# Optimization experiments

Hardware: AMD Instinct MI355X
Metric: run time of the kernel (lower is better)

The kernel has to match this reference:

```python
import jax, jax.numpy as jnp
import numpy as np

N_NODES = 100000


def _sage_conv(x, edge_index, W_l, W_r, b):
    # PyG SAGEConv (mean aggr): out_i = lin_l(mean_{j in N(i)} x_j) + lin_r(x_i)
    src, dst = edge_index[0], edge_index[1]
    msg = x[src]  # [E, d] gather
    agg_sum = jax.ops.segment_sum(msg, dst, num_segments=N_NODES)  # [N, d]
    deg = jax.ops.segment_sum(jnp.ones((src.shape[0],), x.dtype), dst, num_segments=N_NODES)
    agg = agg_sum / jnp.maximum(deg, 1.0)[:, None]  # mean aggregation
    return agg @ W_l.T + b + x @ W_r.T


def setup_inputs() -> dict:
    key = jax.random.key(0)
    k = jax.random.split(key, 8)
    d_in, hidden, out = 64, 128, 128
    x = jax.random.normal(k[0], (N_NODES, d_in), dtype=jnp.float32)
    edge_index = jax.random.randint(k[1], (2, 1600000), 0, N_NODES, dtype=jnp.int64)
    s1 = 1.0 / np.sqrt(d_in)
    s2 = 1.0 / np.sqrt(hidden)
    return {
        "x": x,
        "edge_index": edge_index,
        "W1_l": jax.random.uniform(k[2], (hidden, d_in), jnp.float32, -s1, s1),
        "W1_r": jax.random.uniform(k[3], (hidden, d_in), jnp.float32, -s1, s1),
        "b1": jnp.zeros((hidden,), jnp.float32),
        "W2_l": jax.random.uniform(k[4], (out, hidden), jnp.float32, -s2, s2),
        "W2_r": jax.random.uniform(k[5], (out, hidden), jnp.float32, -s2, s2),
        "b2": jnp.zeros((out,), jnp.float32),
    }


def reference(x, edge_index, W1_l, W1_r, b1, W2_l, W2_r, b2):
    h = jax.nn.relu(_sage_conv(x, edge_index, W1_l, W1_r, b1))
    return _sage_conv(h, edge_index, W2_l, W2_r, b2)
```

## Files before the change

kernel.cpp:

```cpp
#include <hip/hip_runtime.h>

#define NN 100000
#define NE 1600000
#define SCAN_BLK 2048

#define BSH 9
#define NBUCK2 ((NN + 511) / 512)
#define CHUNK 8192
#define NCHK ((NE + CHUNK - 1) / CHUNK)
#define L2T (NBUCK2 * NCHK)
#define NSTRIP (NN / 32)
#define NG128 (NN / 16)

using bf16x8 = __attribute__((ext_vector_type(8))) short;
using f32x16 = __attribute__((ext_vector_type(16))) float;

__device__ __forceinline__ unsigned short f2bf(float f) {
    unsigned u = __float_as_uint(f);
    u += 0x7FFFu + ((u >> 16) & 1u);
    return (unsigned short)(u >> 16);
}
__device__ __forceinline__ float bf2f(unsigned short h) {
    return __uint_as_float(((unsigned)h) << 16);
}

__global__ __launch_bounds__(256) void hist2_kernel(const int* __restrict__ dst,
                                                    int* __restrict__ histm) {
    __shared__ int lh[256];
    int blk = blockIdx.x, tid = threadIdx.x;
    lh[tid] = 0;
    __syncthreads();
    int base = blk * CHUNK;
#pragma unroll
    for (int t = 0; t < CHUNK / 256; t++) {
        int e = base + t * 256 + tid;
        if (e < NE) atomicAdd(&lh[dst[e] >> BSH], 1);
    }
    __syncthreads();
    if (tid < NBUCK2) histm[tid * NCHK + blk] = lh[tid];
}

__global__ __launch_bounds__(256) void scan1_kernel(int* __restrict__ data,
                                                    int* __restrict__ bsums, int L) {
    __shared__ int s[256];
    int bid = blockIdx.x, tid = threadIdx.x;
    int base = bid * SCAN_BLK + tid * 8;
    int v[8];
    int sum = 0;
#pragma unroll
    for (int t = 0; t < 8; t++) {
        int idx = base + t;
        v[t] = (idx < L) ? data[idx] : 0;
        sum += v[t];
    }
    s[tid] = sum;
    __syncthreads();
    for (int off = 1; off < 256; off <<= 1) {
        int val = (tid >= off) ? s[tid - off] : 0;
        __syncthreads();
        s[tid] += val;
        __syncthreads();
    }
    int excl = s[tid] - sum;
    if (tid == 255) bsums[bid] = s[255];
    int run = excl;
#pragma unroll
    for (int t = 0; t < 8; t++) {
        int idx = base + t;
        if (idx < L) data[idx] = run;
        run += v[t];
    }
}

__global__ __launch_bounds__(64) void scan2_kernel(int* __restrict__ bsums, int n) {
    int tid = threadIdx.x;
    int orig = (tid < n) ? bsums[tid] : 0;
    int v = orig;
    for (int off = 1; off < 64; off <<= 1) {
        int nb = __shfl_up(v, off, 64);
        if (tid >= off) v += nb;
    }
    if (tid < n) bsums[tid] = v - orig;
}

__global__ __launch_bounds__(256) void scan_add_kernel(int* __restrict__ data,
                                                       const int* __restrict__ bsums, int L) {
    int i = blockIdx.x * 256 + threadIdx.x;
    if (i < L) data[i] += bsums[i / SCAN_BLK];
}

__global__ __launch_bounds__(256) void scatter2_kernel(const int* __restrict__ src,
                                                       const int* __restrict__ dst,
                                                       const int* __restrict__ histm,
                                                       int* __restrict__ tmp) {
    __shared__ int lcur[256];
    int blk = blockIdx.x, tid = threadIdx.x;
    if (tid < NBUCK2) lcur[tid] = histm[tid * NCHK + blk];
    __syncthreads();
    int base = blk * CHUNK;
#pragma unroll
    for (int t = 0; t < CHUNK / 256; t++) {
        int e = base + t * 256 + tid;
        if (e < NE) {
            int d = dst[e];
            int p = atomicAdd(&lcur[d >> BSH], 1);
            tmp[p] = src[e] | ((d & 511) << 17);
        }
    }
}

__global__ __launch_bounds__(256) void count_place_kernel(const int* __restrict__ histm,
                                                          const int* __restrict__ tmp,
                                                          int* __restrict__ rowptr,
                                                          int* __restrict__ esrc) {
    __shared__ int cnt[512];
    __shared__ int s[256];
    int b = blockIdx.x, tid = threadIdx.x;
    int beg = histm[b * NCHK];
    int end = (b == NBUCK2 - 1) ? NE : histm[(b + 1) * NCHK];

    cnt[tid] = 0; cnt[tid + 256] = 0;
    __syncthreads();
    for (int e = beg + tid; e < end; e += 256)
        atomicAdd(&cnt[tmp[e] >> 17], 1);
    __syncthreads();

    int c0 = cnt[2 * tid], c1 = cnt[2 * tid + 1];
    int sum = c0 + c1;
    s[tid] = sum;
    __syncthreads();
    for (int off = 1; off < 256; off <<= 1) {
        int val = (tid >= off) ? s[tid - off] : 0;
        __syncthreads();
        s[tid] += val;
        __syncthreads();
    }
    int o0 = beg + s[tid] - sum;
    int o1 = o0 + c0;
    cnt[2 * tid] = o0;
    cnt[2 * tid + 1] = o1;
    int node0 = (b << BSH) + 2 * tid;
    if (node0 < NN)     rowptr[node0]     = o0;
    if (node0 + 1 < NN) rowptr[node0 + 1] = o1;
    if (b == 0 && tid == 0) rowptr[NN] = NE;
    __syncthreads();

    for (int e = beg + tid; e < end; e += 256) {
        int v = tmp[e];
        int p = atomicAdd(&cnt[v >> 17], 1);
        esrc[p] = v & 0x1FFFF;
    }
}

__global__ __launch_bounds__(256) void cvt_kernel(const float* __restrict__ in,
                                                  unsigned short* __restrict__ out, int n4) {
    int i = blockIdx.x * 256 + threadIdx.x;
    if (i < n4) {
        float4 f = ((const float4*)in)[i];
        ((ushort4*)out)[i] = make_ushort4(f2bf(f.x), f2bf(f.y), f2bf(f.z), f2bf(f.w));
    }
}

__global__ __launch_bounds__(256) void agg64_kernel(const unsigned short* __restrict__ feat,
                                                    const int* __restrict__ rowptr,
                                                    const int* __restrict__ esrc,
                                                    unsigned short* __restrict__ agg) {
    int node = blockIdx.x * 4 + (threadIdx.x >> 6);
    int lane = threadIdx.x & 63;
    int es = lane >> 3;
    int fi = lane & 7;
    int beg = rowptr[node], end = rowptr[node + 1];

    float ax[8];
#pragma unroll
    for (int i = 0; i < 8; i++) ax[i] = 0.0f;

    int e = beg;
    for (; e + 15 < end; e += 16) {
        int sA = esrc[e + es];
        int sB = esrc[e + 8 + es];
        bf16x8 uA = *(const bf16x8*)(feat + (size_t)sA * 64 + fi * 8);
        bf16x8 uB = *(const bf16x8*)(feat + (size_t)sB * 64 + fi * 8);
#pragma unroll
        for (int i = 0; i < 8; i++)
            ax[i] += bf2f((unsigned short)uA[i]) + bf2f((unsigned short)uB[i]);
    }
    if (e + 7 < end) {
        int s = esrc[e + es];
        bf16x8 u = *(const bf16x8*)(feat + (size_t)s * 64 + fi * 8);
#pragma unroll
        for (int i = 0; i < 8; i++) ax[i] += bf2f((unsigned short)u[i]);
        e += 8;
    }
    if (es < end - e) {
        int s = esrc[e + es];
        bf16x8 u = *(const bf16x8*)(feat + (size_t)s * 64 + fi * 8);
#pragma unroll
        for (int i = 0; i < 8; i++) ax[i] += bf2f((unsigned short)u[i]);
    }

#pragma unroll
    for (int i = 0; i < 8; i++) {
        ax[i] += __shfl_xor(ax[i], 8);
        ax[i] += __shfl_xor(ax[i], 16);
        ax[i] += __shfl_xor(ax[i], 32);
    }
    if (es == 0) {
        float inv = 1.0f / fmaxf((float)(end - beg), 1.0f);
        bf16x8 o;
#pragma unroll
        for (int i = 0; i < 8; i++) o[i] = (short)f2bf(ax[i] * inv);
        *(bf16x8*)(agg + (size_t)node * 64 + fi * 8) = o;
    }
}

__global__ __launch_bounds__(256) void agg128_split_kernel(
    const unsigned short* __restrict__ hbT,
    const int* __restrict__ rowptr,
    const int* __restrict__ esrc,
    unsigned short* __restrict__ agg) {
    int b = blockIdx.x;
    int c = b & 7;
    int g = b >> 3;
    int tid = threadIdx.x;
    int w = tid >> 6;
    int lane = tid & 63;
    int node = g * 16 + w * 4 + (lane >> 4);
    int es = (lane >> 1) & 7;
    int fi = lane & 1;
    int beg = rowptr[node], end = rowptr[node + 1];

    const unsigned short* tab = hbT + (size_t)c * NN * 16;

    float ax[8];
#pragma unroll
    for (int i = 0; i < 8; i++) ax[i] = 0.0f;

    int e = beg + es;
    for (; e + 8 < end; e += 16) {
        int s0 = esrc[e];
        int s1 = esrc[e + 8];
        bf16x8 u0 = *(const bf16x8*)(tab + (size_t)s0 * 16 + fi * 8);
        bf16x8 u1 = *(const bf16x8*)(tab + (size_t)s1 * 16 + fi * 8);
#pragma unroll
        for (int i = 0; i < 8; i++)
            ax[i] += bf2f((unsigned short)u0[i]) + bf2f((unsigned short)u1[i]);
    }
    if (e < end) {
        int s0 = esrc[e];
        bf16x8 u0 = *(const bf16x8*)(tab + (size_t)s0 * 16 + fi * 8);
#pragma unroll
        for (int i = 0; i < 8; i++) ax[i] += bf2f((unsigned short)u0[i]);
    }

#pragma unroll
    for (int i = 0; i < 8; i++) {
        ax[i] += __shfl_xor(ax[i], 2);
        ax[i] += __shfl_xor(ax[i], 4);
        ax[i] += __shfl_xor(ax[i], 8);
    }
    if (es == 0) {
        float inv = 1.0f / fmaxf((float)(end - beg), 1.0f);
        bf16x8 o;
#pragma unroll
        for (int i = 0; i < 8; i++) o[i] = (short)f2bf(ax[i] * inv);
        *(bf16x8*)(agg + (size_t)node * 128 + c * 16 + fi * 8) = o;
    }
}

template <int K, bool RELU, bool OUTBF, bool A2SPLIT, bool OUTSPLIT>
__global__ __launch_bounds__(256) void gemm_mfma_kernel(
    const unsigned short* __restrict__ A1,
    const unsigned short* __restrict__ A2,
    const unsigned short* __restrict__ Wa,
    const unsigned short* __restrict__ Wb,
    const float* __restrict__ bias,
    void* __restrict__ outv) {
    int strip = blockIdx.x * 4 + (threadIdx.x >> 6);
    if (strip >= NSTRIP) return;
    const int lane = threadIdx.x & 63;
    const int m = lane & 31;
    const int half = lane >> 5;
    const int base = strip * 32;

    f32x16 acc[4];
#pragma unroll
    for (int nb = 0; nb < 4; ++nb)
#pragma unroll
        for (int r = 0; r < 16; ++r) acc[nb][r] = 0.0f;

    const unsigned short* ar1 = A1 + (size_t)(base + m) * K + half * 8;
#pragma unroll
    for (int kc = 0; kc < K; kc += 16) {
        bf16x8 a = *(const bf16x8*)(ar1 + kc);
#pragma unroll
        for (int nb = 0; nb < 4; ++nb) {
            bf16x8 b = *(const bf16x8*)(Wa + (size_t)(nb * 32 + m) * K + kc + half * 8);
            acc[nb] = __builtin_amdgcn_mfma_f32_32x32x16_bf16(a, b, acc[nb], 0, 0, 0);
        }
    }
#pragma unroll
    for (int kc = 0; kc < K; kc += 16) {
        bf16x8 a;
        if (A2SPLIT) {
            int off = kc + half * 8;
            a = *(const bf16x8*)(A2 + (size_t)(off >> 4) * NN * 16 +
                                 (size_t)(base + m) * 16 + (off & 15));
        } else {
            a = *(const bf16x8*)(A2 + (size_t)(base + m) * K + half * 8 + kc);
        }
#pragma unroll
        for (int nb = 0; nb < 4; ++nb) {
            bf16x8 b = *(const bf16x8*)(Wb + (size_t)(nb * 32 + m) * K + kc + half * 8);
            acc[nb] = __builtin_amdgcn_mfma_f32_32x32x16_bf16(a, b, acc[nb], 0, 0, 0);
        }
    }

#pragma unroll
    for (int nb = 0; nb < 4; ++nb) {
        int j = nb * 32 + m;
        float bz = bias[j];
#pragma unroll
        for (int r = 0; r < 16; ++r) {
            int row = (r & 3) + 8 * (r >> 2) + 4 * half;
            float v = acc[nb][r] + bz;
            if (RELU) v = fmaxf(v, 0.0f);
            if (OUTSPLIT) {
                size_t idx = (size_t)(j >> 4) * NN * 16 + (size_t)(base + row) * 16 + (j & 15);
                ((unsigned short*)outv)[idx] = f2bf(v);
            } else {
                size_t idx = (size_t)(base + row) * 128 + j;
                if (OUTBF) ((unsigned short*)outv)[idx] = f2bf(v);
                else       ((float*)outv)[idx] = v;
            }
        }
    }
}

extern "C" void kernel_launch(void* const* d_in, const int* in_sizes, int n_in,
                              void* d_out, int out_size, void* d_ws, size_t ws_size,
                              hipStream_t stream) {
    const float* x   = (const float*)d_in[0];
    const int*   ei  = (const int*)d_in[1];
    const float* W1l = (const float*)d_in[2];
    const float* W1r = (const float*)d_in[3];
    const float* b1  = (const float*)d_in[4];
    const float* W2l = (const float*)d_in[5];
    const float* W2r = (const float*)d_in[6];
    const float* b2  = (const float*)d_in[7];
    float* out = (float*)d_out;

    const int* src = ei;
    const int* dst = ei + NE;

    char* ws = (char*)d_ws;
    int* rowptr = (int*)ws;
    int* esrc   = (int*)(ws + 401408);
    unsigned short* aggB = (unsigned short*)(ws + 6803456);
    unsigned short* xb   = aggB + (size_t)NN * 64;
    char* E = ws + 32403456;
    unsigned short* hbT = (unsigned short*)E;
    int* tmp   = (int*)E;
    int* histm = (int*)(E + 6400000);
    int* bsums = (int*)(E + 6560000);
    unsigned short* W1lb = (unsigned short*)d_out;
    unsigned short* W1rb = W1lb + 128 * 64;
    unsigned short* W2lb = (unsigned short*)ws;
    unsigned short* W2rb = W2lb + 128 * 128;

    const int GB  = (NSTRIP + 3) / 4;
    const int NSB2 = (L2T + SCAN_BLK - 1) / SCAN_BLK;

    hist2_kernel<<<NCHK, 256, 0, stream>>>(dst, histm);
    scan1_kernel<<<NSB2, 256, 0, stream>>>(histm, bsums, L2T);
    scan2_kernel<<<1, 64, 0, stream>>>(bsums, NSB2);
    scan_add_kernel<<<(L2T + 255) / 256, 256, 0, stream>>>(histm, bsums, L2T);
    scatter2_kernel<<<NCHK, 256, 0, stream>>>(src, dst, histm, tmp);
    count_place_kernel<<<NBUCK2, 256, 0, stream>>>(histm, tmp, rowptr, esrc);

    cvt_kernel<<<(NN * 64 / 4 + 255) / 256, 256, 0, stream>>>(x, xb, NN * 64 / 4);
    cvt_kernel<<<(128 * 64 / 4 + 255) / 256, 256, 0, stream>>>(W1l, W1lb, 128 * 64 / 4);
    cvt_kernel<<<(128 * 64 / 4 + 255) / 256, 256, 0, stream>>>(W1r, W1rb, 128 * 64 / 4);

    agg64_kernel<<<NN / 4, 256, 0, stream>>>(xb, rowptr, esrc, aggB);
    gemm_mfma_kernel<64, true, true, false, true><<<GB, 256, 0, stream>>>(
        aggB, xb, W1lb, W1rb, b1, hbT);

    agg128_split_kernel<<<NG128 * 8, 256, 0, stream>>>(hbT, rowptr, esrc, aggB);
    cvt_kernel<<<(128 * 128 / 4 + 255) / 256, 256, 0, stream>>>(W2l, W2lb, 128 * 128 / 4);
    cvt_kernel<<<(128 * 128 / 4 + 255) / 256, 256, 0, stream>>>(W2r, W2rb, 128 * 128 / 4);
    gemm_mfma_kernel<128, false, false, true, false><<<GB, 256, 0, stream>>>(
        aggB, hbT, W2lb, W2rb, b2, out);
}
```

Before: 349.9 us.

## Assign one wavefront per node in split agg128 and store aggregate in split layout

The second-layer aggregation kernel now maps one wavefront per node instead of four nodes per wavefront. Each of 32 lane pairs handles a strided subset of edges, and the partial sums are reduced across the full wave. The aggregate is written in the same chunked (split) layout as the hidden table, and the second GEMM gains an A1SPLIT option to read it. This makes the stores contiguous per chunk and spreads each node's edges over more lanes. The trade-off is 4x more blocks and wasted lanes for low-degree nodes, since average degree is about 16.

```diff
diff --git a/kernel.cpp b/kernel.cpp
--- a/kernel.cpp
+++ b/kernel.cpp
@@ -10,7 +10,6 @@
 #define NCHK ((NE + CHUNK - 1) / CHUNK)
 #define L2T (NBUCK2 * NCHK)
 #define NSTRIP (NN / 32)
-#define NG128 (NN / 16)
 
 using bf16x8 = __attribute__((ext_vector_type(8))) short;
 using f32x16 = __attribute__((ext_vector_type(16))) float;
@@ -218,39 +217,25 @@
     const unsigned short* __restrict__ hbT,
     const int* __restrict__ rowptr,
     const int* __restrict__ esrc,
-    unsigned short* __restrict__ agg) {
-    int b = blockIdx.x;
-    int c = b & 7;
-    int g = b >> 3;
-    int tid = threadIdx.x;
-    int w = tid >> 6;
-    int lane = tid & 63;
-    int node = g * 16 + w * 4 + (lane >> 4);
-    int es = (lane >> 1) & 7;
+    unsigned short* __restrict__ aggT) {
+    int c = blockIdx.x & 7;
+    int node = (blockIdx.x >> 3) * 4 + (threadIdx.x >> 6);
+    int lane = threadIdx.x & 63;
+    int es = lane >> 1;
     int fi = lane & 1;
     int beg = rowptr[node], end = rowptr[node + 1];
 
-    const unsigned short* tab = hbT + (size_t)c * NN * 16;
+    const unsigned short* tab = hbT + (size_t)c * NN * 16 + fi * 8;
 
     float ax[8];
 #pragma unroll
     for (int i = 0; i < 8; i++) ax[i] = 0.0f;
 
-    int e = beg + es;
-    for (; e + 8 < end; e += 16) {
-        int s0 = esrc[e];
-        int s1 = esrc[e + 8];
-        bf16x8 u0 = *(const bf16x8*)(tab + (size_t)s0 * 16 + fi * 8);
-        bf16x8 u1 = *(const bf16x8*)(tab + (size_t)s1 * 16 + fi * 8);
-#pragma unroll
-        for (int i = 0; i < 8; i++)
-            ax[i] += bf2f((unsigned short)u0[i]) + bf2f((unsigned short)u1[i]);
-    }
-    if (e < end) {
-        int s0 = esrc[e];
-        bf16x8 u0 = *(const bf16x8*)(tab + (size_t)s0 * 16 + fi * 8);
-#pragma unroll
-        for (int i = 0; i < 8; i++) ax[i] += bf2f((unsigned short)u0[i]);
+    for (int e = beg + es; e < end; e += 32) {
+        int s = esrc[e];
+        bf16x8 u = *(const bf16x8*)(tab + (size_t)s * 16);
+#pragma unroll
+        for (int i = 0; i < 8; i++) ax[i] += bf2f((unsigned short)u[i]);
     }
 
 #pragma unroll
@@ -258,17 +243,19 @@
         ax[i] += __shfl_xor(ax[i], 2);
         ax[i] += __shfl_xor(ax[i], 4);
         ax[i] += __shfl_xor(ax[i], 8);
+        ax[i] += __shfl_xor(ax[i], 16);
+        ax[i] += __shfl_xor(ax[i], 32);
     }
     if (es == 0) {
         float inv = 1.0f / fmaxf((float)(end - beg), 1.0f);
         bf16x8 o;
 #pragma unroll
         for (int i = 0; i < 8; i++) o[i] = (short)f2bf(ax[i] * inv);
-        *(bf16x8*)(agg + (size_t)node * 128 + c * 16 + fi * 8) = o;
-    }
-}
-
-template <int K, bool RELU, bool OUTBF, bool A2SPLIT, bool OUTSPLIT>
+        *(bf16x8*)(aggT + (size_t)c * NN * 16 + (size_t)node * 16 + fi * 8) = o;
+    }
+}
+
+template <int K, bool RELU, bool OUTBF, bool A1SPLIT, bool A2SPLIT, bool OUTSPLIT>
 __global__ __launch_bounds__(256) void gemm_mfma_kernel(
     const unsigned short* __restrict__ A1,
     const unsigned short* __restrict__ A2,
@@ -289,10 +276,16 @@
 #pragma unroll
         for (int r = 0; r < 16; ++r) acc[nb][r] = 0.0f;
 
-    const unsigned short* ar1 = A1 + (size_t)(base + m) * K + half * 8;
 #pragma unroll
     for (int kc = 0; kc < K; kc += 16) {
-        bf16x8 a = *(const bf16x8*)(ar1 + kc);
+        bf16x8 a;
+        if (A1SPLIT) {
+            int off = kc + half * 8;
+            a = *(const bf16x8*)(A1 + (size_t)(off >> 4) * NN * 16 +
+                                 (size_t)(base + m) * 16 + (off & 15));
+        } else {
+            a = *(const bf16x8*)(A1 + (size_t)(base + m) * K + half * 8 + kc);
+        }
 #pragma unroll
         for (int nb = 0; nb < 4; ++nb) {
             bf16x8 b = *(const bf16x8*)(Wa + (size_t)(nb * 32 + m) * K + kc + half * 8);
@@ -383,12 +376,12 @@
     cvt_kernel<<<(128 * 64 / 4 + 255) / 256, 256, 0, stream>>>(W1r, W1rb, 128 * 64 / 4);
 
     agg64_kernel<<<NN / 4, 256, 0, stream>>>(xb, rowptr, esrc, aggB);
-    gemm_mfma_kernel<64, true, true, false, true><<<GB, 256, 0, stream>>>(
+    gemm_mfma_kernel<64, true, true, false, false, true><<<GB, 256, 0, stream>>>(
         aggB, xb, W1lb, W1rb, b1, hbT);
 
-    agg128_split_kernel<<<NG128 * 8, 256, 0, stream>>>(hbT, rowptr, esrc, aggB);
+    agg128_split_kernel<<<(NN / 4) * 8, 256, 0, stream>>>(hbT, rowptr, esrc, aggB);
     cvt_kernel<<<(128 * 128 / 4 + 255) / 256, 256, 0, stream>>>(W2l, W2lb, 128 * 128 / 4);
     cvt_kernel<<<(128 * 128 / 4 + 255) / 256, 256, 0, stream>>>(W2r, W2rb, 128 * 128 / 4);
-    gemm_mfma_kernel<128, false, false, true, false><<<GB, 256, 0, stream>>>(
+    gemm_mfma_kernel<128, false, false, true, true, false><<<GB, 256, 0, stream>>>(
         aggB, hbT, W2lb, W2rb, b2, out);
 }
```

Result: slower. 587.2 us (+67.8%).
